# Kernel optimization log

Hardware: AMD Instinct MI355X
Metric: run time of the kernel (lower is better)

The kernel has to match this reference:

```python
import jax, jax.numpy as jnp
import numpy as np

B, IN, C, HID, EMB = 1024, 512, 128, 128, 32


def setup_inputs() -> dict:
    key = jax.random.key(0)
    ks = jax.random.split(key, 9)
    s1 = 1.0 / np.sqrt(IN)
    s2 = 1.0 / np.sqrt(HID)
    return {
        "x": jax.random.normal(ks[0], (B, IN), jnp.float32),
        "pos_W1": jax.random.normal(ks[1], (C, IN, HID), jnp.float32) * s1,
        "pos_b1": jax.random.normal(ks[2], (C, HID), jnp.float32) * s1,
        "pos_W2": jax.random.normal(ks[3], (C, HID, EMB), jnp.float32) * s2,
        "pos_b2": jax.random.normal(ks[4], (C, EMB), jnp.float32) * s2,
        "neg_W1": jax.random.normal(ks[5], (C, IN, HID), jnp.float32) * s1,
        "neg_b1": jax.random.normal(ks[6], (C, HID), jnp.float32) * s1,
        "neg_W2": jax.random.normal(ks[7], (C, HID, EMB), jnp.float32) * s2,
        "neg_b2": jax.random.normal(ks[8], (C, EMB), jnp.float32) * s2,
    }


def _bank(x, W1, b1, W2, b2):
    # x: [B, IN]; W1: [C, IN, HID]; W2: [C, HID, EMB]
    h = jnp.einsum("bi,cih->bch", x, W1) + b1          # [B, C, HID]
    h = jax.nn.relu(h)                                  # dropout is identity in eval
    out = jnp.einsum("bch,che->bce", h, W2) + b2        # [B, C, EMB]
    return jnp.transpose(out, (0, 2, 1))                # [B, EMB, C]


def reference(x, pos_W1, pos_b1, pos_W2, pos_b2, neg_W1, neg_b1, neg_W2, neg_b2):
    pos = _bank(x, pos_W1, pos_b1, pos_W2, pos_b2)
    neg = _bank(x, neg_W1, neg_b1, neg_W2, neg_b2)
    return pos, neg
```

## Files before the change

### kernel.cpp

```cpp
#include <hip/hip_runtime.h>
#include <hip/hip_bf16.h>

#define B_TOT  1024
#define IN_DIM 512
#define C_DIM  128
#define HID    128
#define EMB    32
#define BK     32
#define NKT    (IN_DIM / BK)

#define WS_W1_STRIDE 65536ull
#define WS_W2_OFF    16777216ull
#define WS_X_OFF     17825792ull
#define WS_TMP_US    18350080ull
#define WS_NEEDED1_B 36700160ull
#define WS_NEEDED2_B 53477376ull

using bf16x8 = __attribute__((ext_vector_type(8))) short;
using f32x4  = __attribute__((ext_vector_type(4))) float;
using f32x2  = __attribute__((ext_vector_type(2))) float;

__device__ __forceinline__ unsigned short f2b(float f) {
    union { __hip_bfloat16 h; unsigned short u; } cv;
    cv.h = __float2bfloat16(f);
    return cv.u;
}
__device__ __forceinline__ float b2f32(unsigned short u) {
    union { unsigned int i; float f; } c;
    c.i = ((unsigned int)u) << 16;
    return c.f;
}
__device__ __forceinline__ unsigned int pack2(float a, float b) {
    return (unsigned int)f2b(a) | ((unsigned int)f2b(b) << 16);
}
__device__ __forceinline__ unsigned long long pack4(float a, float b, float c, float d) {
    return (unsigned long long)pack2(a, b) | ((unsigned long long)pack2(c, d) << 32);
}
__device__ __forceinline__ bf16x8 ld16(const unsigned short* p) {
    return *(const bf16x8*)p;
}
__device__ __forceinline__ void g2l16(const unsigned short* g, unsigned short* l) {
    __builtin_amdgcn_global_load_lds(
        (const __attribute__((address_space(1))) unsigned int*)(g),
        (__attribute__((address_space(3))) unsigned int*)(l), 16, 0, 0);
}

__global__ __launch_bounds__(256) void prepass(
    const float* __restrict__ x,
    const float* __restrict__ pW1, const float* __restrict__ pW2,
    const float* __restrict__ nW1, const float* __restrict__ nW2,
    unsigned short* __restrict__ ws)
{
    __shared__ unsigned short img[4096];
    const int blk     = blockIdx.x;
    const int pair    = blk >> 2;
    const int quarter = blk & 3;
    const int bank    = pair >> 7;
    const int c       = pair & 127;
    const int t       = threadIdx.x;

    const float* W1c = (bank ? nW1 : pW1) + (size_t)c * IN_DIM * HID;
    const float* W2c = (bank ? nW2 : pW2) + (size_t)c * HID * EMB;

    if (quarter == 0) {
        int e0 = (t & 7) * 4, h0 = (t >> 3) * 4;
        const float* src = &W2c[(size_t)h0 * EMB + e0];
        f32x4 L0 = *(const f32x4*)(src + 0 * EMB);
        f32x4 L1 = *(const f32x4*)(src + 1 * EMB);
        f32x4 L2 = *(const f32x4*)(src + 2 * EMB);
        f32x4 L3 = *(const f32x4*)(src + 3 * EMB);
        unsigned short* dst = ws + WS_W2_OFF + (size_t)pair * 4096;
#pragma unroll
        for (int j = 0; j < 4; ++j) {
            int e = e0 + j;
            int idx = (h0 >> 5) * 1024 + (e >> 4) * 512 +
                      ((((h0 & 31) >> 3) * 16 + (e & 15)) * 8) + (h0 & 7);
            *(unsigned long long*)&dst[idx] = pack4(L0[j], L1[j], L2[j], L3[j]);
        }
    }

#pragma unroll
    for (int q = 0; q < 4; ++q) {
        const int kt = quarter * 4 + q;
        const float* Wk = W1c + (size_t)kt * BK * HID;
        {
            int k0 = (t >> 5) * 4;
            int h0 = (t & 31) * 4;
            const float* src = &Wk[(size_t)k0 * HID + h0];
            f32x4 L0 = *(const f32x4*)(src + 0 * HID);
            f32x4 L1 = *(const f32x4*)(src + 1 * HID);
            f32x4 L2 = *(const f32x4*)(src + 2 * HID);
            f32x4 L3 = *(const f32x4*)(src + 3 * HID);
#pragma unroll
            for (int j = 0; j < 4; ++j) {
                int h = h0 + j;
                int idx = (h >> 4) * 512 +
                          (((k0 >> 3) * 16 + (h & 15)) * 8) + (k0 & 7);
                *(unsigned long long*)&img[idx] = pack4(L0[j], L1[j], L2[j], L3[j]);
            }
        }
        __syncthreads();
        unsigned short* dst = ws + (size_t)pair * WS_W1_STRIDE + (size_t)kt * 4096;
        *(bf16x8*)&dst[t * 16]     = *(const bf16x8*)&img[t * 16];
        *(bf16x8*)&dst[t * 16 + 8] = *(const bf16x8*)&img[t * 16 + 8];
        __syncthreads();
    }

    {
        const int row = blk;
        if (t < 128) {
            int k0 = t * 4;
            f32x4 v = *(const f32x4*)&x[(size_t)row * IN_DIM + k0];
            size_t idx = WS_X_OFF + (size_t)(row >> 7) * 65536 +
                         (size_t)(k0 >> 5) * 4096 + (size_t)((row & 127) >> 4) * 512 +
                         ((((k0 & 31) >> 3) * 16 + (row & 15)) * 8) + (k0 & 7);
            *(unsigned long long*)&ws[idx] = pack4(v[0], v[1], v[2], v[3]);
        }
    }
}

__global__ __launch_bounds__(512, 2) void bank_main(
    const float* __restrict__ pb1, const float* __restrict__ pb2,
    const float* __restrict__ nb1, const float* __restrict__ nb2,
    const unsigned short* __restrict__ ws,
    unsigned short* __restrict__ tmp,
    float* __restrict__ out)
{
    __shared__ unsigned short smem[32768];

    const int p     = blockIdx.x;
    const int xcd   = p & 7;
    const int rank  = p >> 3;
    const int cg    = rank & 7;
    const int btile = (rank >> 3) & 3;
    const int bank  = rank >> 5;
    const int c0    = xcd * 16 + cg * 2;
    const int bbase = btile * 256;

    const int t    = threadIdx.x;
    const int wave = t >> 6;
    const int lane = t & 63;
    const int lr   = lane & 15;
    const int lkg  = lane >> 4;
    const int wm   = wave >> 1;
    const int wn   = wave & 1;

    const unsigned short* xsrc0 = ws + WS_X_OFF + (size_t)(btile * 2) * 65536;
    const unsigned short* xsrc1 = xsrc0 + 65536;
    const unsigned short* wsrc0 = ws + (size_t)(bank * 128 + c0) * WS_W1_STRIDE;
    const unsigned short* wsrc1 = wsrc0 + WS_W1_STRIDE;

    f32x4 acc[4][8];
#pragma unroll
    for (int mi = 0; mi < 4; ++mi)
#pragma unroll
        for (int ni = 0; ni < 8; ++ni) acc[mi][ni] = (f32x4){0.f, 0.f, 0.f, 0.f};

#define STAGE(KT, SEL)                                                          \
    {                                                                           \
        g2l16(xsrc0 + (KT) * 4096 + t * 8, &smem[(SEL) * 8192 + t * 8]);        \
        g2l16(xsrc1 + (KT) * 4096 + t * 8, &smem[(SEL) * 8192 + 4096 + t * 8]); \
        g2l16(wsrc0 + (KT) * 4096 + t * 8, &smem[16384 + (SEL) * 8192 + t * 8]);\
        g2l16(wsrc1 + (KT) * 4096 + t * 8,                                      \
              &smem[16384 + (SEL) * 8192 + 4096 + t * 8]);                      \
    }

    STAGE(0, 0);
    __syncthreads();

    for (int kt = 0; kt < NKT; ++kt) {
        const int sel = kt & 1;
        if (kt < NKT - 1) STAGE(kt + 1, sel ^ 1);

        const unsigned short* Xb = &smem[sel * 8192 + (wm >> 1) * 4096 +
                                         (wm & 1) * 2048 + lane * 8];
        const unsigned short* Wb = &smem[16384 + sel * 8192 + wn * 4096 + lane * 8];
        bf16x8 af[4], bfr[8];
#pragma unroll
        for (int mi = 0; mi < 4; ++mi) af[mi] = ld16(Xb + mi * 512);
#pragma unroll
        for (int ni = 0; ni < 8; ++ni) bfr[ni] = ld16(Wb + ni * 512);

        __builtin_amdgcn_s_setprio(1);
#pragma unroll
        for (int mi = 0; mi < 4; ++mi)
#pragma unroll
            for (int ni = 0; ni < 8; ++ni)
                acc[mi][ni] = __builtin_amdgcn_mfma_f32_16x16x32_bf16(
                    af[mi], bfr[ni], acc[mi][ni], 0, 0, 0);
        __builtin_amdgcn_s_setprio(0);
        __syncthreads();
    }
#undef STAGE

    const int cw   = c0 + wn;
    const int pw   = bank * 128 + cw;
    const float* b1c = (bank ? nb1 : pb1) + cw * HID;
    const float* b2c = (bank ? nb2 : pb2) + cw * EMB;
    float b1v[8];
#pragma unroll
    for (int ni = 0; ni < 8; ++ni) b1v[ni] = b1c[ni * 16 + lr];
    float b2v[2];
#pragma unroll
    for (int ei = 0; ei < 2; ++ei) b2v[ei] = b2c[ei * 16 + lr];

    const unsigned short* w2base = ws + WS_W2_OFF + (size_t)pw * 4096 + lane * 8;
    bf16x8 w2f[2][4];
#pragma unroll
    for (int k2 = 0; k2 < 4; ++k2)
#pragma unroll
        for (int ei = 0; ei < 2; ++ei)
            w2f[ei][k2] = ld16(w2base + k2 * 1024 + ei * 512);

    unsigned short* slot = &smem[wave * 4096];
    f32x4 acc2[4][2];
#pragma unroll
    for (int m2 = 0; m2 < 4; ++m2)
#pragma unroll
        for (int ei = 0; ei < 2; ++ei) acc2[m2][ei] = (f32x4){0.f, 0.f, 0.f, 0.f};

#pragma unroll
    for (int ch = 0; ch < 2; ++ch) {
#pragma unroll
        for (int mi = 0; mi < 4; ++mi) {
#pragma unroll
            for (int nq = 0; nq < 4; ++nq) {
                int ni = ch * 4 + nq;
                int lh = nq * 16 + lr;
#pragma unroll
                for (int j = 0; j < 4; ++j) {
                    int r = mi * 16 + lkg * 4 + j;
                    float v = fmaxf(acc[mi][ni][j] + b1v[ni], 0.f);
                    slot[r * 64 + ((((lh >> 3) & 7) ^ (r & 7)) << 3) + (lh & 7)] = f2b(v);
                }
            }
        }
#pragma unroll
        for (int kk = 0; kk < 2; ++kk) {
            int k2 = ch * 2 + kk;
            bf16x8 a2[4];
#pragma unroll
            for (int m2 = 0; m2 < 4; ++m2) {
                int r = m2 * 16 + lr;
                a2[m2] = ld16(&slot[r * 64 + (((kk * 4 + lkg) ^ (r & 7)) << 3)]);
            }
#pragma unroll
            for (int m2 = 0; m2 < 4; ++m2)
#pragma unroll
                for (int ei = 0; ei < 2; ++ei)
                    acc2[m2][ei] = __builtin_amdgcn_mfma_f32_16x16x32_bf16(
                        a2[m2], w2f[ei][k2], acc2[m2][ei], 0, 0, 0);
        }
    }

    if (tmp != nullptr) {
        unsigned short* tb = tmp + (size_t)pw * (B_TOT * EMB);
#pragma unroll
        for (int m2 = 0; m2 < 4; ++m2) {
#pragma unroll
            for (int ei = 0; ei < 2; ++ei) {
                int e = ei * 16 + lr;
#pragma unroll
                for (int j = 0; j < 4; ++j) {
                    int brow = bbase + wm * 64 + m2 * 16 + lkg * 4 + j;
                    tb[(size_t)brow * EMB + e] = f2b(acc2[m2][ei][j] + b2v[ei]);
                }
            }
        }
    } else {
        float* outb = out + (size_t)bank * B_TOT * EMB * C_DIM;
#pragma unroll
        for (int m2 = 0; m2 < 4; ++m2) {
#pragma unroll
            for (int ei = 0; ei < 2; ++ei) {
                int e = ei * 16 + lr;
#pragma unroll
                for (int j = 0; j < 4; ++j) {
                    int brow = bbase + wm * 64 + m2 * 16 + lkg * 4 + j;
                    outb[((size_t)brow * EMB + e) * C_DIM + cw] = acc2[m2][ei][j] + b2v[ei];
                }
            }
        }
    }
}

#define LP 1026
__global__ __launch_bounds__(256, 2) void untranspose(
    const unsigned short* __restrict__ tmp, float* __restrict__ out)
{
    __shared__ float lds[16 * LP];
    const int blk   = blockIdx.x;
    const int bank  = blk >> 8;
    const int cg    = (blk >> 5) & 7;
    const int chunk = blk & 31;
    const size_t beBase = (size_t)chunk * 1024;
    const int t = threadIdx.x;

#pragma unroll
    for (int ci = 0; ci < 16; ++ci) {
        const int pair = bank * 128 + cg * 16 + ci;
        unsigned long long q = *(const unsigned long long*)
            &tmp[(size_t)pair * (B_TOT * EMB) + beBase + t * 4];
#pragma unroll
        for (int j = 0; j < 4; ++j)
            lds[ci * LP + t * 4 + j] = b2f32((unsigned short)(q >> (16 * j)));
    }
    __syncthreads();

    float* outb = out + (size_t)bank * (B_TOT * EMB * C_DIM);
#pragma unroll
    for (int w = 0; w < 16; ++w) {
        int be = w * 64 + (t >> 2);
        int c4 = t & 3;
        f32x4 o;
#pragma unroll
        for (int j = 0; j < 4; ++j) o[j] = lds[(c4 * 4 + j) * LP + be];
        *(f32x4*)&outb[(beBase + be) * C_DIM + cg * 16 + c4 * 4] = o;
    }
}
#undef LP

#define XS_LD 68
#define W1_LD 68
#define HS_LD 132
#define W2_LD 132
__device__ __forceinline__ bf16x8 load8u(const unsigned short* p) {
    union { unsigned long long q[2]; bf16x8 v; } u;
    u.q[0] = *(const unsigned long long*)(p);
    u.q[1] = *(const unsigned long long*)(p + 4);
    return u.v;
}
__global__ __launch_bounds__(256, 2) void bank_fallback(
    const float* __restrict__ x,
    const float* __restrict__ pW1, const float* __restrict__ pb1,
    const float* __restrict__ pW2, const float* __restrict__ pb2,
    const float* __restrict__ nW1, const float* __restrict__ nb1,
    const float* __restrict__ nW2, const float* __restrict__ nb2,
    float* __restrict__ out)
{
    __shared__ unsigned short Xs [128][XS_LD];
    __shared__ unsigned short W1T[HID][W1_LD];
    __shared__ unsigned short Hs [128][HS_LD];
    __shared__ unsigned short W2T[EMB][W2_LD];
    int p = blockIdx.x;
    int xcd = p & 7, rank = p >> 3;
    int c = xcd * 16 + (rank & 15);
    int btile = (rank >> 4) & 7;
    int bank = rank >> 7;
    int bbase = btile * 128;
    const float* W1c = (bank ? nW1 : pW1) + (size_t)c * IN_DIM * HID;
    const float* b1c = (bank ? nb1 : pb1) + c * HID;
    const float* W2c = (bank ? nW2 : pW2) + (size_t)c * HID * EMB;
    const float* b2c = (bank ? nb2 : pb2) + c * EMB;
    float* outb = out + (size_t)bank * B_TOT * EMB * C_DIM;
    int t = threadIdx.x, wave = t >> 6, lane = t & 63;
    int lr = lane & 15, lkg = lane >> 4, wm = wave >> 1, wn = wave & 1;
    {
        int e0 = (t & 7) * 4, h0 = (t >> 3) * 4;
        f32x4 L0 = *(const f32x4*)&W2c[(h0 + 0) * EMB + e0];
        f32x4 L1 = *(const f32x4*)&W2c[(h0 + 1) * EMB + e0];
        f32x4 L2 = *(const f32x4*)&W2c[(h0 + 2) * EMB + e0];
        f32x4 L3 = *(const f32x4*)&W2c[(h0 + 3) * EMB + e0];
#pragma unroll
        for (int j = 0; j < 4; ++j)
            *(unsigned long long*)&W2T[e0 + j][h0] = pack4(L0[j], L1[j], L2[j], L3[j]);
    }
    float b1v[4];
#pragma unroll
    for (int ni = 0; ni < 4; ++ni) b1v[ni] = b1c[wn * 64 + ni * 16 + lr];
    float b2v[2];
#pragma unroll
    for (int ei = 0; ei < 2; ++ei) b2v[ei] = b2c[ei * 16 + lr];
    f32x4 acc[4][4];
#pragma unroll
    for (int mi = 0; mi < 4; ++mi)
#pragma unroll
        for (int ni = 0; ni < 4; ++ni) acc[mi][ni] = (f32x4){0.f, 0.f, 0.f, 0.f};
    for (int kt = 0; kt < 8; ++kt) {
        int kb = kt * 64;
#pragma unroll
        for (int w8 = 0; w8 < 8; ++w8) {
            int f = w8 * 256 + t;
            int row = f >> 4, col = (f & 15) * 4;
            f32x4 v = *(const f32x4*)&x[(size_t)(bbase + row) * IN_DIM + kb + col];
            *(unsigned long long*)&Xs[row][col] = pack4(v[0], v[1], v[2], v[3]);
        }
#pragma unroll
        for (int g = 0; g < 2; ++g) {
            int s = g * 256 + t;
            int k0 = (s >> 5) * 4, h0 = (s & 31) * 4;
            const float* src = &W1c[(size_t)(kb + k0) * HID + h0];
            f32x4 L0 = *(const f32x4*)(src + 0 * HID);
            f32x4 L1 = *(const f32x4*)(src + 1 * HID);
            f32x4 L2 = *(const f32x4*)(src + 2 * HID);
            f32x4 L3 = *(const f32x4*)(src + 3 * HID);
#pragma unroll
            for (int j = 0; j < 4; ++j)
                *(unsigned long long*)&W1T[h0 + j][k0] = pack4(L0[j], L1[j], L2[j], L3[j]);
        }
        __syncthreads();
#pragma unroll
        for (int ki = 0; ki < 2; ++ki) {
            int kcol = ki * 32 + lkg * 8;
            bf16x8 af[4], bfr[4];
#pragma unroll
            for (int mi = 0; mi < 4; ++mi) af[mi] = load8u(&Xs[wm * 64 + mi * 16 + lr][kcol]);
#pragma unroll
            for (int ni = 0; ni < 4; ++ni) bfr[ni] = load8u(&W1T[wn * 64 + ni * 16 + lr][kcol]);
#pragma unroll
            for (int mi = 0; mi < 4; ++mi)
#pragma unroll
                for (int ni = 0; ni < 4; ++ni)
                    acc[mi][ni] = __builtin_amdgcn_mfma_f32_16x16x32_bf16(
                        af[mi], bfr[ni], acc[mi][ni], 0, 0, 0);
        }
        __syncthreads();
    }
#pragma unroll
    for (int mi = 0; mi < 4; ++mi) {
        int row = wm * 64 + mi * 16 + lkg * 4;
#pragma unroll
        for (int ni = 0; ni < 4; ++ni) {
            int col = wn * 64 + ni * 16 + lr;
#pragma unroll
            for (int j = 0; j < 4; ++j)
                Hs[row + j][col] = f2b(fmaxf(acc[mi][ni][j] + b1v[ni], 0.f));
        }
    }
    __syncthreads();
    f32x4 acc2[2][2];
#pragma unroll
    for (int m2 = 0; m2 < 2; ++m2)
#pragma unroll
        for (int ei = 0; ei < 2; ++ei) acc2[m2][ei] = (f32x4){0.f, 0.f, 0.f, 0.f};
    int rb = wave * 32;
#pragma unroll
    for (int k2 = 0; k2 < 4; ++k2) {
        int kcol = k2 * 32 + lkg * 8;
        bf16x8 a2[2], b2f[2];
#pragma unroll
        for (int m2 = 0; m2 < 2; ++m2) a2[m2] = load8u(&Hs[rb + m2 * 16 + lr][kcol]);
#pragma unroll
        for (int ei = 0; ei < 2; ++ei) b2f[ei] = load8u(&W2T[ei * 16 + lr][kcol]);
#pragma unroll
        for (int m2 = 0; m2 < 2; ++m2)
#pragma unroll
            for (int ei = 0; ei < 2; ++ei)
                acc2[m2][ei] = __builtin_amdgcn_mfma_f32_16x16x32_bf16(
                    a2[m2], b2f[ei], acc2[m2][ei], 0, 0, 0);
    }
#pragma unroll
    for (int m2 = 0; m2 < 2; ++m2)
#pragma unroll
        for (int ei = 0; ei < 2; ++ei) {
            int e = ei * 16 + lr;
#pragma unroll
            for (int j = 0; j < 4; ++j) {
                int brow = bbase + rb + m2 * 16 + lkg * 4 + j;
                outb[((size_t)brow * EMB + e) * C_DIM + c] = acc2[m2][ei][j] + b2v[ei];
            }
        }
}

extern "C" void kernel_launch(void* const* d_in, const int* in_sizes, int n_in,
                              void* d_out, int out_size, void* d_ws, size_t ws_size,
                              hipStream_t stream) {
    const float* x   = (const float*)d_in[0];
    const float* pW1 = (const float*)d_in[1];
    const float* pb1 = (const float*)d_in[2];
    const float* pW2 = (const float*)d_in[3];
    const float* pb2 = (const float*)d_in[4];
    const float* nW1 = (const float*)d_in[5];
    const float* nb1 = (const float*)d_in[6];
    const float* nW2 = (const float*)d_in[7];
    const float* nb2 = (const float*)d_in[8];
    float* out = (float*)d_out;

    if (ws_size >= WS_NEEDED2_B) {
        unsigned short* ws  = (unsigned short*)d_ws;
        unsigned short* tmp = (unsigned short*)d_ws + WS_TMP_US;
        prepass<<<dim3(1024), dim3(256), 0, stream>>>(x, pW1, pW2, nW1, nW2, ws);
        bank_main<<<dim3(512), dim3(512), 0, stream>>>(pb1, pb2, nb1, nb2, ws, tmp, out);
        untranspose<<<dim3(512), dim3(256), 0, stream>>>(tmp, out);
    } else if (ws_size >= WS_NEEDED1_B) {
        unsigned short* ws = (unsigned short*)d_ws;
        prepass<<<dim3(1024), dim3(256), 0, stream>>>(x, pW1, pW2, nW1, nW2, ws);
        bank_main<<<dim3(512), dim3(512), 0, stream>>>(pb1, pb2, nb1, nb2, ws,
                                                       (unsigned short*)nullptr, out);
    } else {
        bank_fallback<<<dim3(2048), dim3(256), 0, stream>>>(
            x, pW1, pb1, pW2, pb2, nW1, nb1, nW2, nb2, out);
    }
}
```

Before: 67.68 us.

## Load W1 fragments directly from global into registers, bypassing LDS

W1 tiles are no longer staged through shared memory. Each wave now reads its own W1 fragments straight from global memory into a double-buffered register set, prefetched one k-step ahead, while only x still goes through LDS. The k-loop is fully unrolled so the two register buffers can alternate. This cuts LDS traffic and LDS write/read instructions for the weights, at the cost of more VGPRs (16 extra bf16x8 vectors) and global load latency that is exposed when one k-step of MFMA work cannot hide it.

```diff
diff --git a/kernel.cpp b/kernel.cpp
--- a/kernel.cpp
+++ b/kernel.cpp
@@ -147,8 +147,8 @@
 
     const unsigned short* xsrc0 = ws + WS_X_OFF + (size_t)(btile * 2) * 65536;
     const unsigned short* xsrc1 = xsrc0 + 65536;
-    const unsigned short* wsrc0 = ws + (size_t)(bank * 128 + c0) * WS_W1_STRIDE;
-    const unsigned short* wsrc1 = wsrc0 + WS_W1_STRIDE;
+    const unsigned short* wsel  = ws + (size_t)(bank * 128 + c0 + wn) * WS_W1_STRIDE
+                                  + lane * 8;
 
     f32x4 acc[4][8];
 #pragma unroll
@@ -156,42 +156,53 @@
 #pragma unroll
         for (int ni = 0; ni < 8; ++ni) acc[mi][ni] = (f32x4){0.f, 0.f, 0.f, 0.f};
 
-#define STAGE(KT, SEL)                                                          \
+#define STAGEX(KT, SEL)                                                         \
     {                                                                           \
         g2l16(xsrc0 + (KT) * 4096 + t * 8, &smem[(SEL) * 8192 + t * 8]);        \
         g2l16(xsrc1 + (KT) * 4096 + t * 8, &smem[(SEL) * 8192 + 4096 + t * 8]); \
-        g2l16(wsrc0 + (KT) * 4096 + t * 8, &smem[16384 + (SEL) * 8192 + t * 8]);\
-        g2l16(wsrc1 + (KT) * 4096 + t * 8,                                      \
-              &smem[16384 + (SEL) * 8192 + 4096 + t * 8]);                      \
-    }
-
-    STAGE(0, 0);
+    }
+
+    bf16x8 B0[8], B1[8];
+
+#define KSTEP(KT, BU, BN, DOPRE)                                                \
+    {                                                                           \
+        if (DOPRE) {                                                            \
+            _Pragma("unroll")                                                   \
+            for (int n = 0; n < 8; ++n)                                         \
+                BN[n] = ld16(wsel + ((KT) + 1) * 4096 + n * 512);               \
+            STAGEX((KT) + 1, ((KT) + 1) & 1);                                   \
+        }                                                                       \
+        const unsigned short* Xb = &smem[((KT) & 1) * 8192 + (wm >> 1) * 4096 + \
+                                         (wm & 1) * 2048 + lane * 8];           \
+        bf16x8 af[4];                                                           \
+        _Pragma("unroll")                                                       \
+        for (int i = 0; i < 4; ++i) af[i] = ld16(Xb + i * 512);                 \
+        __builtin_amdgcn_s_setprio(1);                                          \
+        _Pragma("unroll")                                                       \
+        for (int mi = 0; mi < 4; ++mi)                                          \
+            _Pragma("unroll")                                                   \
+            for (int ni = 0; ni < 8; ++ni)                                      \
+                acc[mi][ni] = __builtin_amdgcn_mfma_f32_16x16x32_bf16(          \
+                    af[mi], BU[ni], acc[mi][ni], 0, 0, 0);                      \
+        __builtin_amdgcn_s_setprio(0);                                          \
+        __syncthreads();                                                        \
+    }
+
+#pragma unroll
+    for (int n = 0; n < 8; ++n) B0[n] = ld16(wsel + n * 512);
+    STAGEX(0, 0);
     __syncthreads();
 
-    for (int kt = 0; kt < NKT; ++kt) {
-        const int sel = kt & 1;
-        if (kt < NKT - 1) STAGE(kt + 1, sel ^ 1);
-
-        const unsigned short* Xb = &smem[sel * 8192 + (wm >> 1) * 4096 +
-                                         (wm & 1) * 2048 + lane * 8];
-        const unsigned short* Wb = &smem[16384 + sel * 8192 + wn * 4096 + lane * 8];
-        bf16x8 af[4], bfr[8];
-#pragma unroll
-        for (int mi = 0; mi < 4; ++mi) af[mi] = ld16(Xb + mi * 512);
-#pragma unroll
-        for (int ni = 0; ni < 8; ++ni) bfr[ni] = ld16(Wb + ni * 512);
-
-        __builtin_amdgcn_s_setprio(1);
-#pragma unroll
-        for (int mi = 0; mi < 4; ++mi)
-#pragma unroll
-            for (int ni = 0; ni < 8; ++ni)
-                acc[mi][ni] = __builtin_amdgcn_mfma_f32_16x16x32_bf16(
-                    af[mi], bfr[ni], acc[mi][ni], 0, 0, 0);
-        __builtin_amdgcn_s_setprio(0);
-        __syncthreads();
-    }
-#undef STAGE
+    KSTEP(0,  B0, B1, 1)  KSTEP(1,  B1, B0, 1)
+    KSTEP(2,  B0, B1, 1)  KSTEP(3,  B1, B0, 1)
+    KSTEP(4,  B0, B1, 1)  KSTEP(5,  B1, B0, 1)
+    KSTEP(6,  B0, B1, 1)  KSTEP(7,  B1, B0, 1)
+    KSTEP(8,  B0, B1, 1)  KSTEP(9,  B1, B0, 1)
+    KSTEP(10, B0, B1, 1)  KSTEP(11, B1, B0, 1)
+    KSTEP(12, B0, B1, 1)  KSTEP(13, B1, B0, 1)
+    KSTEP(14, B0, B1, 1)  KSTEP(15, B1, B0, 0)
+#undef KSTEP
+#undef STAGEX
 
     const int cw   = c0 + wn;
     const int pw   = bank * 128 + cw;
```

Result: slower. 73.44 us (+8.5%).
